# Kernel tuning notes

Hardware: AMD Instinct MI355X
Metric: run time of the kernel (lower is better)

The kernel has to match this reference:

```python
import jax, jax.numpy as jnp
import numpy as np

B, D, H, C, T = 65536, 512, 256, 100, 10
EPS = 0.01  # halt_epsilon


def setup_inputs() -> dict:
    key = jax.random.key(0)
    ks = jax.random.split(key, 10)
    sD = 1.0 / np.sqrt(D)
    sH = 1.0 / np.sqrt(H)
    return {
        "x": jax.random.normal(ks[0], (B, D), dtype=jnp.float32),
        # GRUCell params (PyTorch layout: rows chunked as [r; z; n])
        "W_ih": jax.random.uniform(ks[1], (3 * H, D), minval=-sD, maxval=sD, dtype=jnp.float32),
        "W_hh": jax.random.uniform(ks[2], (3 * H, H), minval=-sH, maxval=sH, dtype=jnp.float32),
        "b_ih": jax.random.uniform(ks[3], (3 * H,), minval=-sH, maxval=sH, dtype=jnp.float32),
        "b_hh": jax.random.uniform(ks[4], (3 * H,), minval=-sH, maxval=sH, dtype=jnp.float32),
        # halting unit
        "W_halt": jax.random.uniform(ks[5], (1, H), minval=-sH, maxval=sH, dtype=jnp.float32),
        "b_halt": jax.random.uniform(ks[6], (1,), minval=-sH, maxval=sH, dtype=jnp.float32),
        # readout
        "W_ro": jax.random.uniform(ks[7], (C, H), minval=-sH, maxval=sH, dtype=jnp.float32),
        "b_ro": jax.random.uniform(ks[8], (C,), minval=-sH, maxval=sH, dtype=jnp.float32),
    }


def _act_forward(x, W_ih, W_hh, b_ih, b_hh, W_halt, b_halt, W_ro, b_ro):
    dt = x.dtype
    thresh = jnp.asarray(1.0 - EPS, dt)
    # x is static across ponder steps -> precompute input projection once
    x_proj = x @ W_ih.T + b_ih                       # [B, 3H]
    xr, xz, xn = jnp.split(x_proj, 3, axis=-1)

    def step(carry, _):
        h, cum, rem, nup, acc = carry
        h_proj = h @ W_hh.T + b_hh                   # [B, 3H]
        hr, hz, hn = jnp.split(h_proj, 3, axis=-1)
        r = jax.nn.sigmoid(xr + hr)
        z = jax.nn.sigmoid(xz + hz)
        n = jnp.tanh(xn + r * hn)
        h_new = (1.0 - z) * n + z * h                # GRUCell update
        halt = jax.nn.sigmoid(h_new @ W_halt.T + b_halt)[:, 0]  # [B]
        logits_t = h_new @ W_ro.T + b_ro             # [B, C]
        still = (cum < thresh).astype(dt)
        new_halt = halt * still
        would = (cum + new_halt > thresh).astype(dt)
        remainder = (1.0 - cum) * would * still
        step_w = new_halt * (1.0 - would) + remainder
        cum2 = cum + step_w
        acc2 = acc + step_w[:, None] * h_new
        return (h_new, cum2, rem + remainder, nup + still, acc2), (h_new, halt, logits_t)

    zB = jnp.zeros((x.shape[0],), dt)
    init = (jnp.zeros((x.shape[0], W_hh.shape[1]), dt), zB, zB, zB,
            jnp.zeros((x.shape[0], W_hh.shape[1]), dt))
    (h, cum, remainders, n_updates, acc), (h_seq, halt_seq, logits_seq) = jax.lax.scan(
        step, init, None, length=T)
    logits = acc @ W_ro.T + b_ro                     # [B, C]
    ponder_cost = n_updates.mean() + remainders.mean()
    # scan stacks on axis 0 (time) -> move to dim 1 as torch.stack(dim=1)
    h_seq = jnp.swapaxes(h_seq, 0, 1)                # [B, T, H]
    halt_seq = jnp.swapaxes(halt_seq, 0, 1)          # [B, T]
    logits_seq = jnp.swapaxes(logits_seq, 0, 1)      # [B, T, C]
    return logits, ponder_cost, n_updates, h_seq, halt_seq, logits_seq


def reference(x, W_ih, W_hh, b_ih, b_hh, W_halt, b_halt, W_ro, b_ro):
    return _act_forward(x, W_ih, W_hh, b_ih, b_hh, W_halt, b_halt, W_ro, b_ro)
```

## Files before the change

kernel.cpp:

```cpp
#include <hip/hip_runtime.h>
#include <cmath>


namespace {
constexpr int B = 65536, D = 512, H = 256, C = 100, T = 10;

constexpr long OUT_LOGITS = 0;
constexpr long OUT_PONDER = (long)B * C;
constexpr long OUT_NUP    = OUT_PONDER + 1;
constexpr long OUT_HSEQ   = OUT_NUP + B;
constexpr long OUT_HALT   = OUT_HSEQ + (long)B * T * H;
constexpr long OUT_LSEQ   = OUT_HALT + (long)B * T;

constexpr long NIH  = 768L * D;
constexpr long NHH  = 768L * H;
constexpr long NAUG = 112L * H;

constexpr long WS_XP   = 0;
constexpr long WS_W16  = WS_XP + (long)B * 768;
constexpr long W_HALV  = 2 * (NIH + NHH + NAUG);
constexpr long WS_HL   = WS_W16 + (W_HALV + 1) / 2;
constexpr long WS_HP4  = WS_HL + (long)B * T;
constexpr long WS_NUPB = WS_HP4 + 4L * B * T;
constexpr long WS_REMB = WS_NUPB + B;
constexpr long WS_H16  = WS_REMB + B;
constexpr long H16_PER_T = 1024L * 32768;

constexpr float SC  = 256.f;
constexpr float ISC = 1.f / 256.f;
constexpr float SB  = 1.f / 65536.f;
}

typedef __attribute__((ext_vector_type(8))) _Float16 h8;
typedef __attribute__((ext_vector_type(4))) _Float16 h4;
typedef __attribute__((ext_vector_type(4))) float f4;

#define MFMA16(A, Bo, Cc) __builtin_amdgcn_mfma_f32_16x16x32_f16(A, Bo, Cc, 0, 0, 0)
#define PROD3(a, Ah, Al, Bh, Bl)                                               \
  a = MFMA16(Al, Bh, a);                                                       \
  a = MFMA16(Ah, Bl, a);                                                       \
  a = MFMA16(Ah, Bh, a);

__device__ __forceinline__ float sigmoidf_(float x) {
  if (x >= 0.f) { return 1.f / (1.f + expf(-x)); }
  float e = expf(x);
  return e / (1.f + e);
}

__device__ __forceinline__ void gload_lds16(const _Float16* g, _Float16* l) {
  __builtin_amdgcn_global_load_lds(
      (const __attribute__((address_space(1))) unsigned int*)g,
      (__attribute__((address_space(3))) unsigned int*)l, 16, 0, 0);
}

__global__ void k_prep(const float* __restrict__ wih_s, const float* __restrict__ whh_s,
                       const float* __restrict__ wro, const float* __restrict__ whalt,
                       _Float16* __restrict__ wr) {
  long idx = (long)blockIdx.x * 256 + threadIdx.x;
  if (idx < NIH) {
    float xs = wih_s[idx] * SC;
    _Float16 h = (_Float16)xs;
    _Float16 l = (_Float16)(xs - (float)h);
    wr[idx] = h; wr[NIH + idx] = l;
  }
  if (idx < NHH) {
    float xs = whh_s[idx] * SC;
    _Float16 h = (_Float16)xs;
    _Float16 l = (_Float16)(xs - (float)h);
    long b = 2 * NIH;
    wr[b + idx] = h; wr[b + NHH + idx] = l;
  }
  if (idx < NAUG) {
    int row = (int)(idx >> 8), k = (int)(idx & 255);
    float x = (row < C) ? wro[row * 256 + k] : ((row == C) ? whalt[k] : 0.f);
    float xs = x * SC;
    _Float16 h = (_Float16)xs;
    _Float16 l = (_Float16)(xs - (float)h);
    long b = 2 * (NIH + NHH);
    wr[b + idx] = h; wr[b + NAUG + idx] = l;
  }
}

__device__ __forceinline__ void stageA16(const float* __restrict__ src,
                                         _Float16* As0, _Float16* As1,
                                         int o) {
#pragma unroll
  for (int i = 0; i < 4; ++i) {
    float4 v = ((const float4*)src)[i];
    float vv[4] = {v.x, v.y, v.z, v.w};
    h4 hh, ll;
#pragma unroll
    for (int c = 0; c < 4; ++c) {
      float sv = vv[c] * SC;
      _Float16 h = (_Float16)sv;
      hh[c] = h;
      ll[c] = (_Float16)(sv - (float)h);
    }
    *(h4*)&As0[o + i * 4] = hh;
    *(h4*)&As1[o + i * 4] = ll;
  }
}

__global__ __launch_bounds__(256, 3) void k_xproj(
    const float* __restrict__ x, const _Float16* __restrict__ wih,
    const float* __restrict__ b_ih, float* __restrict__ xpt) {
  __shared__ __align__(16) _Float16 As0[128 * 40], As1[128 * 40];
  __shared__ __align__(16) _Float16 Bs[2][192 * 32];
  const int tid = threadIdx.x;
  const int w = tid >> 6, l = tid & 63;
  const int lr = l & 15, lq = l >> 4;
  const int bid = blockIdx.x;
  const int gid = (bid & 7) * 256 + (bid >> 3);
  const int c0 = (gid & 3) * 64;
  const int rb = (gid >> 2) * 128;

  f4 acc[8][3];
#pragma unroll
  for (int i = 0; i < 8; ++i)
#pragma unroll
    for (int g = 0; g < 3; ++g) acc[i][g] = (f4)0.f;

  for (int kc = 0; kc < 16; ++kc) {
    const int k0 = kc * 32;
    __syncthreads();
    {
      const int row = tid >> 1, kk0 = (tid & 1) * 16;
      stageA16(x + (long)(rb + row) * D + k0 + kk0, As0, As1, row * 40 + kk0);
    }
#pragma unroll
    for (int j = 0; j < 6; ++j) {
      int chunk = w * 6 + j;
      int plane = chunk / 12;
      int rem = chunk - plane * 12;
      int scol = rem * 16 + (l >> 2);
      int kq = l & 3;
      int gcol = (scol >> 6) * 256 + c0 + (scol & 63);
      gload_lds16(wih + (long)plane * NIH + (long)gcol * D + k0 + kq * 8,
                  &Bs[plane][rem * 512]);
    }
    __syncthreads();
    h8 Bh[3], Bl[3];
#pragma unroll
    for (int g = 0; g < 3; ++g) {
      Bh[g] = *(const h8*)&Bs[0][(g * 64 + w * 16 + lr) * 32 + lq * 8];
      Bl[g] = *(const h8*)&Bs[1][(g * 64 + w * 16 + lr) * 32 + lq * 8];
    }
#pragma unroll
    for (int i = 0; i < 8; ++i) {
      h8 Ah = *(const h8*)&As0[(i * 16 + lr) * 40 + lq * 8];
      h8 Al = *(const h8*)&As1[(i * 16 + lr) * 40 + lq * 8];
#pragma unroll
      for (int g = 0; g < 3; ++g) { PROD3(acc[i][g], Ah, Al, Bh[g], Bl[g]); }
    }
  }
  const int ch = c0 + w * 16 + lr;
  const int strip = gid & 3;
  float bi[3] = {b_ih[ch], b_ih[256 + ch], b_ih[512 + ch]};
  const long xoff = (long)(lq * 256 + w * 64 + lr * 4);
#pragma unroll
  for (int i = 0; i < 8; ++i) {
    const long t4s = (long)((gid >> 2) * 2 + (i >> 2)) * 4 + strip;
#pragma unroll
    for (int g = 0; g < 3; ++g) {
      float4 v = make_float4(fmaf(acc[i][g][0], SB, bi[g]),
                             fmaf(acc[i][g][1], SB, bi[g]),
                             fmaf(acc[i][g][2], SB, bi[g]),
                             fmaf(acc[i][g][3], SB, bi[g]));
      *(float4*)&xpt[((t4s * 3 + g) * 4 + (i & 3)) * 1024 + xoff] = v;
    }
  }
}

__global__ __launch_bounds__(256, 4) void k_gru(
    const _Float16* __restrict__ whh, const float* __restrict__ xpt,
    const float* __restrict__ b_hh, const float* __restrict__ w_halt,
    float* __restrict__ out, _Float16* __restrict__ h16,
    float* __restrict__ hp4, int t) {
  __shared__ __align__(16) char uSmem[32768];
  _Float16* As0 = (_Float16*)uSmem;
  _Float16* As1 = (_Float16*)(uSmem + 4096);
  _Float16* Bs0 = (_Float16*)(uSmem + 8192);
  _Float16* Bs1 = (_Float16*)(uSmem + 20480);
  float*    hseqS = (float*)uSmem;
  _Float16* h16S  = (_Float16*)(uSmem + 16384);
  __shared__ float lds_hp[64][4];
  const int tid = threadIdx.x;
  const int w = tid >> 6, l = tid & 63;
  const int lr = l & 15, lq = l >> 4;
  const int bid = blockIdx.x;
  const int gid = (bid & 7) * 512 + (bid >> 3);
  const int strip = gid & 3;
  const int c0 = strip * 64;
  const int rb = (gid >> 2) * 64;
  const long tilebase = (long)(rb >> 6) * 32768;
  const int ch = c0 + w * 16 + lr;
  const int kc_h = ch >> 5;

  f4 acc[4][3];
  float ho[4][4];
  float xnv[4][4];
  const long t4s = (long)(gid >> 2) * 4 + strip;
  const long xoff = (long)(lq * 256 + w * 64 + lr * 4);
#pragma unroll
  for (int i = 0; i < 4; ++i) {
    float4 vr = *(const float4*)&xpt[((t4s * 3 + 0) * 4 + i) * 1024 + xoff];
    float4 vz = *(const float4*)&xpt[((t4s * 3 + 1) * 4 + i) * 1024 + xoff];
    float4 vn = *(const float4*)&xpt[((t4s * 3 + 2) * 4 + i) * 1024 + xoff];
    acc[i][0][0] = vr.x * 65536.f; acc[i][0][1] = vr.y * 65536.f;
    acc[i][0][2] = vr.z * 65536.f; acc[i][0][3] = vr.w * 65536.f;
    acc[i][1][0] = vz.x * 65536.f; acc[i][1][1] = vz.y * 65536.f;
    acc[i][1][2] = vz.z * 65536.f; acc[i][1][3] = vz.w * 65536.f;
    xnv[i][0] = vn.x; xnv[i][1] = vn.y; xnv[i][2] = vn.z; xnv[i][3] = vn.w;
    acc[i][2] = (f4)0.f;
#pragma unroll
    for (int reg = 0; reg < 4; ++reg) ho[i][reg] = 0.f;
  }

  if (t > 0) {
    const _Float16* h16r = h16 + (long)(t - 1) * H16_PER_T + tilebase;
    for (int kc = 0; kc < 8; ++kc) {
      const int k0 = kc * 32;
      __syncthreads();
#pragma unroll
      for (int j = 0; j < 2; ++j) {
        int c = w * 2 + j;
        int plane = c >> 2;
        int cc = c & 3;
        gload_lds16(h16r + (long)kc * 4096 + plane * 2048 + cc * 512 + l * 8,
                    (plane ? As1 : As0) + cc * 512);
      }
#pragma unroll
      for (int j = 0; j < 6; ++j) {
        int chunk = w * 6 + j;
        int plane = chunk / 12;
        int rem = chunk - plane * 12;
        int scol = rem * 16 + (l >> 2);
        int kq = l & 3;
        int gcol = (scol >> 6) * 256 + c0 + (scol & 63);
        gload_lds16(whh + (long)plane * NHH + (long)gcol * H + k0 + kq * 8,
                    (plane ? Bs1 : Bs0) + rem * 512);
      }
      __syncthreads();
      h8 Bh[3], Bl[3];
#pragma unroll
      for (int g = 0; g < 3; ++g) {
        Bh[g] = *(const h8*)&Bs0[(g * 64 + w * 16 + lr) * 32 + lq * 8];
        Bl[g] = *(const h8*)&Bs1[(g * 64 + w * 16 + lr) * 32 + lq * 8];
      }
#pragma unroll
      for (int i = 0; i < 4; ++i) {
        h8 Ah = *(const h8*)&As0[(i * 16 + lr) * 32 + lq * 8];
        h8 Al = *(const h8*)&As1[(i * 16 + lr) * 32 + lq * 8];
#pragma unroll
        for (int g = 0; g < 3; ++g) { PROD3(acc[i][g], Ah, Al, Bh[g], Bl[g]); }
      }
      if (kc == kc_h) {
#pragma unroll
        for (int i = 0; i < 4; ++i)
#pragma unroll
          for (int reg = 0; reg < 4; ++reg) {
            int rloc = i * 16 + lq * 4 + reg;
            ho[i][reg] = ((float)As0[rloc * 32 + (ch & 31)] +
                          (float)As1[rloc * 32 + (ch & 31)]) * ISC;
          }
      }
    }
  }

  const float bhr = b_hh[ch], bhz = b_hh[256 + ch], bhn = b_hh[512 + ch];
  const float whv = w_halt[ch];
  float hvv[4][4];
#pragma unroll
  for (int i = 0; i < 4; ++i)
#pragma unroll
    for (int reg = 0; reg < 4; ++reg) {
      float rr = sigmoidf_(fmaf(acc[i][0][reg], SB, bhr));
      float zz = sigmoidf_(fmaf(acc[i][1][reg], SB, bhz));
      float nn = tanhf(xnv[i][reg] + rr * fmaf(acc[i][2][reg], SB, bhn));
      hvv[i][reg] = (1.f - zz) * nn + zz * ho[i][reg];
    }

  __syncthreads();

  const int kcl = w >> 1;
  const int kk = (w & 1) * 16 + lr;
#pragma unroll
  for (int i = 0; i < 4; ++i)
#pragma unroll
    for (int reg = 0; reg < 4; ++reg) {
      const int rloc = i * 16 + lq * 4 + reg;
      const float hv = hvv[i][reg];
      hseqS[rloc * 64 + w * 16 + lr] = hv;
      float sv = hv * SC;
      _Float16 hi = (_Float16)sv;
      _Float16 lo = (_Float16)(sv - (float)hi);
      h16S[(kcl * 2 + 0) * 2048 + rloc * 32 + kk] = hi;
      h16S[(kcl * 2 + 1) * 2048 + rloc * 32 + kk] = lo;
      float p = hv * whv;
#pragma unroll
      for (int m = 1; m < 16; m <<= 1) p += __shfl_xor(p, m, 64);
      if (lr == 0) lds_hp[rloc][w] = p;
    }
  __syncthreads();

#pragma unroll
  for (int k = 0; k < 4; ++k) {
    int cid = k * 256 + tid;
    int row = cid >> 4, ch16 = cid & 15;
    *(float4*)&out[OUT_HSEQ + (long)(rb + row) * (T * H) + (long)t * H + c0 + ch16 * 4] =
        *(const float4*)&hseqS[row * 64 + ch16 * 4];
  }
  {
    _Float16* dst = h16 + (long)t * H16_PER_T + tilebase + (long)(2 * strip) * 4096;
#pragma unroll
    for (int k = 0; k < 4; ++k) {
      int cid = k * 256 + tid;
      *(float4*)&dst[cid * 8] = *(const float4*)&h16S[cid * 8];
    }
  }
  if (tid < 64)
    hp4[((long)t * 4 + strip) * B + rb + tid] =
        ((lds_hp[tid][0] + lds_hp[tid][1]) + (lds_hp[tid][2] + lds_hp[tid][3]));
}

__global__ __launch_bounds__(256, 4) void k_lseq(
    const _Float16* __restrict__ h16, const _Float16* __restrict__ waug,
    const float* __restrict__ b_ro, float* __restrict__ lseq) {
  __shared__ __align__(16) _Float16 As[128 * 32];
  __shared__ __align__(16) _Float16 Bs[112 * 32];
  const int tid = threadIdx.x;
  const int w = tid >> 6, l = tid & 63;
  const int lr = l & 15, lq = l >> 4;
  const int t = blockIdx.x >> 9;
  const int btile = blockIdx.x & 511;
  const _Float16* h16r = h16 + (long)t * H16_PER_T + (long)btile * 65536;

  f4 acc[2][7];
#pragma unroll
  for (int i = 0; i < 2; ++i)
#pragma unroll
    for (int j = 0; j < 7; ++j) acc[i][j] = (f4)0.f;

  for (int kc = 0; kc < 8; ++kc) {
    const int k0 = kc * 32;
    __syncthreads();
#pragma unroll
    for (int j = 0; j < 2; ++j) {
      int c = w * 2 + j;
      gload_lds16(h16r + (long)(c >> 2) * 32768 + (long)kc * 4096 + (c & 3) * 512 + l * 8,
                  &As[c * 512]);
    }
#pragma unroll
    for (int j = 0; j < 2; ++j) {
      int chunk = w + j * 4;
      if (chunk < 7) {
        int scol = chunk * 16 + (l >> 2);
        int kq = l & 3;
        gload_lds16(waug + (long)scol * H + k0 + kq * 8, &Bs[chunk * 512]);
      }
    }
    __syncthreads();
    h8 Af[2];
#pragma unroll
    for (int i = 0; i < 2; ++i)
      Af[i] = *(const h8*)&As[(w * 32 + i * 16 + lr) * 32 + lq * 8];
#pragma unroll
    for (int j = 0; j < 7; ++j) {
      h8 Bf = *(const h8*)&Bs[(j * 16 + lr) * 32 + lq * 8];
#pragma unroll
      for (int i = 0; i < 2; ++i) acc[i][j] = MFMA16(Af[i], Bf, acc[i][j]);
    }
  }
#pragma unroll
  for (int j = 0; j < 7; ++j) {
    const int col = j * 16 + lr;
    if (col < C) {
      const float br = b_ro[col];
#pragma unroll
      for (int i = 0; i < 2; ++i)
#pragma unroll
        for (int reg = 0; reg < 4; ++reg) {
          long b = (long)btile * 128 + w * 32 + i * 16 + lq * 4 + reg;
          lseq[(b * T + t) * C + col] = fmaf(acc[i][j][reg], SB, br);
        }
    }
  }
}

__global__ void k_act(const float* __restrict__ hp4, const float* __restrict__ b_halt,
                      float* __restrict__ out, float* __restrict__ swb,
                      float* __restrict__ nupb, float* __restrict__ remb) {
  const long b = (long)blockIdx.x * 256 + threadIdx.x;
  const float bh = b_halt[0];
  float cum = 0.f, rem = 0.f, nu = 0.f;
#pragma unroll
  for (int t = 0; t < T; ++t) {
    float v = bh + hp4[((long)t * 4 + 0) * B + b] + hp4[((long)t * 4 + 1) * B + b] +
              hp4[((long)t * 4 + 2) * B + b] + hp4[((long)t * 4 + 3) * B + b];
    float halt = sigmoidf_(v);
    out[OUT_HALT + b * T + t] = halt;
    float still = (cum < 0.99f) ? 1.f : 0.f;
    float nh = halt * still;
    float would = ((cum + nh) > 0.99f) ? 1.f : 0.f;
    float rema = (1.f - cum) * would * still;
    float swv = nh * (1.f - would) + rema;
    cum += swv; rem += rema; nu += still;
    swb[b * T + t] = swv;
  }
  nupb[b] = nu; remb[b] = rem;
}

__global__ void k_logits(const float* __restrict__ lseq, const float* __restrict__ swb,
                         const float* __restrict__ b_ro, const float* __restrict__ nupb,
                         float* __restrict__ out) {
  const long b = blockIdx.x;
  const int tid = threadIdx.x;
  if (tid < C) {
    float br = b_ro[tid];
    float s = br;
#pragma unroll
    for (int t = 0; t < T; ++t) {
      float sw = swb[b * T + t];
      s = fmaf(sw, lseq[(b * T + t) * C + tid] - br, s);
    }
    out[OUT_LOGITS + b * C + tid] = s;
  } else if (tid == C) {
    out[OUT_NUP + b] = nupb[b];
  }
}

__global__ void k_ponder(const float* __restrict__ nupb, const float* __restrict__ remb,
                         float* __restrict__ out) {
  __shared__ float sm[4];
  float s = 0.f;
  for (int i = threadIdx.x; i < B; i += 256) s += nupb[i] + remb[i];
#pragma unroll
  for (int m = 1; m < 64; m <<= 1) s += __shfl_xor(s, m, 64);
  int w = threadIdx.x >> 6;
  if ((threadIdx.x & 63) == 0) sm[w] = s;
  __syncthreads();
  if (threadIdx.x == 0)
    out[OUT_PONDER] = (sm[0] + sm[1] + sm[2] + sm[3]) * (1.f / (float)B);
}

extern "C" void kernel_launch(void* const* d_in, const int* in_sizes, int n_in,
                              void* d_out, int out_size, void* d_ws, size_t ws_size,
                              hipStream_t stream) {
  const float* x      = (const float*)d_in[0];
  const float* W_ih   = (const float*)d_in[1];
  const float* W_hh   = (const float*)d_in[2];
  const float* b_ih   = (const float*)d_in[3];
  const float* b_hh   = (const float*)d_in[4];
  const float* W_halt = (const float*)d_in[5];
  const float* b_halt = (const float*)d_in[6];
  const float* W_ro   = (const float*)d_in[7];
  const float* b_ro   = (const float*)d_in[8];
  float* out = (float*)d_out;
  float* ws  = (float*)d_ws;

  float* xpt       = ws + WS_XP;
  _Float16* w16    = (_Float16*)(ws + WS_W16);
  _Float16* wih16  = w16;
  _Float16* whh16  = w16 + 2 * NIH;
  _Float16* waug16 = w16 + 2 * (NIH + NHH);
  float* swb  = ws + WS_HL;
  float* hp4  = ws + WS_HP4;
  float* nupb = ws + WS_NUPB;
  float* remb = ws + WS_REMB;
  _Float16* h16 = (_Float16*)(ws + WS_H16);

  k_prep<<<(int)((NIH + 255) / 256), 256, 0, stream>>>(W_ih, W_hh, W_ro, W_halt, w16);
  k_xproj<<<2048, 256, 0, stream>>>(x, wih16, b_ih, xpt);
  for (int t = 0; t < T; ++t)
    k_gru<<<4096, 256, 0, stream>>>(whh16, xpt, b_hh, W_halt, out, h16, hp4, t);
  k_lseq<<<512 * T, 256, 0, stream>>>(h16, waug16, b_ro, out + OUT_LSEQ);
  k_act<<<B / 256, 256, 0, stream>>>(hp4, b_halt, out, swb, nupb, remb);
  k_logits<<<B, 128, 0, stream>>>(out + OUT_LSEQ, swb, b_ro, nupb, out);
  k_ponder<<<1, 256, 0, stream>>>(nupb, remb, out);
}
```

Before: 1.993 ms.

## Double-buffer hidden-state tiles in LDS and load W_hh fragments directly to registers

The GRU step kernel now double-buffers the h16 A-tiles in shared memory, prefetching the next k-chunk while computing the current one. It uses raw s_barrier and manual vmcnt waits in place of two __syncthreads per iteration. The W_hh B operands are read straight from global memory into registers instead of being staged through LDS. The aim is to cut barrier stalls and LDS traffic, at the risk of uncoalesced, redundant global weight reads and fragile hand-written wait counts.

```diff
diff --git a/kernel.cpp b/kernel.cpp
--- a/kernel.cpp
+++ b/kernel.cpp
@@ -177,10 +177,7 @@
     float* __restrict__ out, _Float16* __restrict__ h16,
     float* __restrict__ hp4, int t) {
   __shared__ __align__(16) char uSmem[32768];
-  _Float16* As0 = (_Float16*)uSmem;
-  _Float16* As1 = (_Float16*)(uSmem + 4096);
-  _Float16* Bs0 = (_Float16*)(uSmem + 8192);
-  _Float16* Bs1 = (_Float16*)(uSmem + 20480);
+  _Float16* AsBuf = (_Float16*)uSmem;
   float*    hseqS = (float*)uSmem;
   _Float16* h16S  = (_Float16*)(uSmem + 16384);
   __shared__ float lds_hp[64][4];
@@ -196,6 +193,9 @@
   const int ch = c0 + w * 16 + lr;
   const int kc_h = ch >> 5;
 
+  const float bhr = b_hh[ch], bhz = b_hh[256 + ch], bhn = b_hh[512 + ch];
+  const float whv = w_halt[ch];
+
   f4 acc[4][3];
   float ho[4][4];
   float xnv[4][4];
@@ -218,39 +218,39 @@
 
   if (t > 0) {
     const _Float16* h16r = h16 + (long)(t - 1) * H16_PER_T + tilebase;
+
+#define STAGE_A(buf, kc_)                                                       \
+    {                                                                           \
+      _Pragma("unroll")                                                         \
+      for (int j = 0; j < 2; ++j) {                                             \
+        int c = w * 2 + j;                                                      \
+        int plane = c >> 2, cc = c & 3;                                         \
+        gload_lds16(h16r + (long)(kc_) * 4096 + plane * 2048 + cc * 512 + l * 8,\
+                    AsBuf + (buf) * 4096 + plane * 2048 + cc * 512);            \
+      }                                                                         \
+    }
+
+    STAGE_A(0, 0);
+    int cur = 0;
+#pragma unroll
     for (int kc = 0; kc < 8; ++kc) {
       const int k0 = kc * 32;
-      __syncthreads();
-#pragma unroll
-      for (int j = 0; j < 2; ++j) {
-        int c = w * 2 + j;
-        int plane = c >> 2;
-        int cc = c & 3;
-        gload_lds16(h16r + (long)kc * 4096 + plane * 2048 + cc * 512 + l * 8,
-                    (plane ? As1 : As0) + cc * 512);
+      __builtin_amdgcn_s_barrier();
+      h8 Bh[3], Bl[3];
+#pragma unroll
+      for (int g = 0; g < 3; ++g) {
+        Bh[g] = *(const h8*)(whh + (long)(g * 256 + ch) * H + k0 + lq * 8);
+        Bl[g] = *(const h8*)(whh + NHH + (long)(g * 256 + ch) * H + k0 + lq * 8);
       }
-#pragma unroll
-      for (int j = 0; j < 6; ++j) {
-        int chunk = w * 6 + j;
-        int plane = chunk / 12;
-        int rem = chunk - plane * 12;
-        int scol = rem * 16 + (l >> 2);
-        int kq = l & 3;
-        int gcol = (scol >> 6) * 256 + c0 + (scol & 63);
-        gload_lds16(whh + (long)plane * NHH + (long)gcol * H + k0 + kq * 8,
-                    (plane ? Bs1 : Bs0) + rem * 512);
-      }
-      __syncthreads();
-      h8 Bh[3], Bl[3];
-#pragma unroll
-      for (int g = 0; g < 3; ++g) {
-        Bh[g] = *(const h8*)&Bs0[(g * 64 + w * 16 + lr) * 32 + lq * 8];
-        Bl[g] = *(const h8*)&Bs1[(g * 64 + w * 16 + lr) * 32 + lq * 8];
-      }
+      __builtin_amdgcn_sched_barrier(0);
+      if (kc < 7) STAGE_A(cur ^ 1, kc + 1);
+      asm volatile("s_waitcnt vmcnt(2)" ::: "memory");
+      __builtin_amdgcn_s_barrier();
+      __builtin_amdgcn_sched_barrier(0);
 #pragma unroll
       for (int i = 0; i < 4; ++i) {
-        h8 Ah = *(const h8*)&As0[(i * 16 + lr) * 32 + lq * 8];
-        h8 Al = *(const h8*)&As1[(i * 16 + lr) * 32 + lq * 8];
+        h8 Ah = *(const h8*)&AsBuf[cur * 4096 + (i * 16 + lr) * 32 + lq * 8];
+        h8 Al = *(const h8*)&AsBuf[cur * 4096 + 2048 + (i * 16 + lr) * 32 + lq * 8];
 #pragma unroll
         for (int g = 0; g < 3; ++g) { PROD3(acc[i][g], Ah, Al, Bh[g], Bl[g]); }
       }
@@ -260,15 +260,15 @@
 #pragma unroll
           for (int reg = 0; reg < 4; ++reg) {
             int rloc = i * 16 + lq * 4 + reg;
-            ho[i][reg] = ((float)As0[rloc * 32 + (ch & 31)] +
-                          (float)As1[rloc * 32 + (ch & 31)]) * ISC;
+            ho[i][reg] = ((float)AsBuf[cur * 4096 + rloc * 32 + (ch & 31)] +
+                          (float)AsBuf[cur * 4096 + 2048 + rloc * 32 + (ch & 31)]) * ISC;
           }
       }
-    }
-  }
-
-  const float bhr = b_hh[ch], bhz = b_hh[256 + ch], bhn = b_hh[512 + ch];
-  const float whv = w_halt[ch];
+      cur ^= 1;
+    }
+#undef STAGE_A
+  }
+
   float hvv[4][4];
 #pragma unroll
   for (int i = 0; i < 4; ++i)
```

Measured after the change: 2.405 ms. +20.7%, slower.

## Fuse first GRU step into input-projection kernel, skipping zero-state matmul

Applied to the files above, without the earlier changes.

Because the initial hidden state is zero, step 0 of the GRU needs no W_hh product, so the xproj kernel now computes h at t=0 directly from its accumulators plus b_hh. It writes h_seq, the fp16 hi/lo split of h, and the halting partial sums, and the step loop starts at t=1. This removes one full k_gru launch and its zero-state matmul. In exchange xproj uses more shared memory (larger union buffer, different As stride), which may lower its occupancy.

```diff
diff --git a/kernel.cpp b/kernel.cpp
--- a/kernel.cpp
+++ b/kernel.cpp
@@ -103,9 +103,18 @@
 
 __global__ __launch_bounds__(256, 3) void k_xproj(
     const float* __restrict__ x, const _Float16* __restrict__ wih,
-    const float* __restrict__ b_ih, float* __restrict__ xpt) {
-  __shared__ __align__(16) _Float16 As0[128 * 40], As1[128 * 40];
-  __shared__ __align__(16) _Float16 Bs[2][192 * 32];
+    const float* __restrict__ b_ih, const float* __restrict__ b_hh,
+    const float* __restrict__ w_halt, float* __restrict__ xpt,
+    float* __restrict__ out, _Float16* __restrict__ h16,
+    float* __restrict__ hp4) {
+  __shared__ __align__(16) char uSmem[45056];
+  _Float16* As0 = (_Float16*)uSmem;
+  _Float16* As1 = (_Float16*)(uSmem + 10240);
+  _Float16* Bs0 = (_Float16*)(uSmem + 20480);
+  _Float16* Bs1 = (_Float16*)(uSmem + 32768);
+  float*    hseqS = (float*)uSmem;
+  _Float16* h16S  = (_Float16*)(uSmem + 16384);
+  __shared__ float lds_hp[128][4];
   const int tid = threadIdx.x;
   const int w = tid >> 6, l = tid & 63;
   const int lr = l & 15, lq = l >> 4;
@@ -136,14 +145,14 @@
       int kq = l & 3;
       int gcol = (scol >> 6) * 256 + c0 + (scol & 63);
       gload_lds16(wih + (long)plane * NIH + (long)gcol * D + k0 + kq * 8,
-                  &Bs[plane][rem * 512]);
+                  (plane ? Bs1 : Bs0) + rem * 512);
     }
     __syncthreads();
     h8 Bh[3], Bl[3];
 #pragma unroll
     for (int g = 0; g < 3; ++g) {
-      Bh[g] = *(const h8*)&Bs[0][(g * 64 + w * 16 + lr) * 32 + lq * 8];
-      Bl[g] = *(const h8*)&Bs[1][(g * 64 + w * 16 + lr) * 32 + lq * 8];
+      Bh[g] = *(const h8*)&Bs0[(g * 64 + w * 16 + lr) * 32 + lq * 8];
+      Bl[g] = *(const h8*)&Bs1[(g * 64 + w * 16 + lr) * 32 + lq * 8];
     }
 #pragma unroll
     for (int i = 0; i < 8; ++i) {
@@ -169,6 +178,59 @@
       *(float4*)&xpt[((t4s * 3 + g) * 4 + (i & 3)) * 1024 + xoff] = v;
     }
   }
+
+  const float bhr = b_hh[ch], bhz = b_hh[256 + ch], bhn = b_hh[512 + ch];
+  const float whv = w_halt[ch];
+  const int kcl = w >> 1;
+  const int kk = (w & 1) * 16 + lr;
+  for (int tl = 0; tl < 2; ++tl) {
+    __syncthreads();
+#pragma unroll
+    for (int ii = 0; ii < 4; ++ii) {
+      const int i = tl * 4 + ii;
+#pragma unroll
+      for (int reg = 0; reg < 4; ++reg) {
+        const int rloc = ii * 16 + lq * 4 + reg;
+        float xrv = fmaf(acc[i][0][reg], SB, bi[0]);
+        float xzv = fmaf(acc[i][1][reg], SB, bi[1]);
+        float xnv = fmaf(acc[i][2][reg], SB, bi[2]);
+        float rr = sigmoidf_(xrv + bhr);
+        float zz = sigmoidf_(xzv + bhz);
+        float nn = tanhf(xnv + rr * bhn);
+        float hv = (1.f - zz) * nn + zz * 0.f;
+        hseqS[rloc * 64 + w * 16 + lr] = hv;
+        float sv = hv * SC;
+        _Float16 hi = (_Float16)sv;
+        _Float16 lo = (_Float16)(sv - (float)hi);
+        h16S[(kcl * 2 + 0) * 2048 + rloc * 32 + kk] = hi;
+        h16S[(kcl * 2 + 1) * 2048 + rloc * 32 + kk] = lo;
+        float p = hv * whv;
+#pragma unroll
+        for (int m = 1; m < 16; m <<= 1) p += __shfl_xor(p, m, 64);
+        if (lr == 0) lds_hp[tl * 64 + rloc][w] = p;
+      }
+    }
+    __syncthreads();
+#pragma unroll
+    for (int k = 0; k < 4; ++k) {
+      int cid = k * 256 + tid;
+      int row = cid >> 4, ch16 = cid & 15;
+      *(float4*)&out[OUT_HSEQ + (long)(rb + tl * 64 + row) * (T * H) + c0 + ch16 * 4] =
+          *(const float4*)&hseqS[row * 64 + ch16 * 4];
+    }
+    {
+      _Float16* dst = h16 + ((long)(rb >> 6) + tl) * 32768 + (long)(2 * strip) * 4096;
+#pragma unroll
+      for (int k = 0; k < 4; ++k) {
+        int cid = k * 256 + tid;
+        *(float4*)&dst[cid * 8] = *(const float4*)&h16S[cid * 8];
+      }
+    }
+  }
+  __syncthreads();
+  if (tid < 128)
+    hp4[(long)strip * B + rb + tid] =
+        (lds_hp[tid][0] + lds_hp[tid][1]) + (lds_hp[tid][2] + lds_hp[tid][3]);
 }
 
 __global__ __launch_bounds__(256, 4) void k_gru(
@@ -470,8 +532,8 @@
   _Float16* h16 = (_Float16*)(ws + WS_H16);
 
   k_prep<<<(int)((NIH + 255) / 256), 256, 0, stream>>>(W_ih, W_hh, W_ro, W_halt, w16);
-  k_xproj<<<2048, 256, 0, stream>>>(x, wih16, b_ih, xpt);
-  for (int t = 0; t < T; ++t)
+  k_xproj<<<2048, 256, 0, stream>>>(x, wih16, b_ih, b_hh, W_halt, xpt, out, h16, hp4);
+  for (int t = 1; t < T; ++t)
     k_gru<<<4096, 256, 0, stream>>>(whh16, xpt, b_hh, W_halt, out, h16, hp4, t);
   k_lseq<<<512 * T, 256, 0, stream>>>(h16, waug16, b_ro, out + OUT_LSEQ);
   k_act<<<B / 256, 256, 0, stream>>>(hp4, b_halt, out, swb, nupb, remb);
```

New measurement: 2.481 ms. 24.5% more time.
